# Performance work log

Hardware: AMD Instinct MI355X
Metric: run time of the kernel (lower is better)

The kernel has to match this reference:

```python
import jax, jax.numpy as jnp
import numpy as np

B, S, D, H = 2, 2048, 1024, 16
HD = D // H  # 64
EPS = 1e-8


def setup_inputs() -> dict:
    key = jax.random.key(0)
    ks = jax.random.split(key, 9)
    hidden_states = jax.random.normal(ks[0], (B, S, D), dtype=jnp.float32)
    # rotary tables: standard RoPE angles over half the head dim
    pos = jnp.arange(S, dtype=jnp.float32)[:, None]
    inv_freq = 1.0 / (10000.0 ** (jnp.arange(0, HD, 2, dtype=jnp.float32) / HD))  # [HD/2]
    ang = pos * inv_freq[None, :]  # [S, HD/2]
    sin = jnp.sin(ang)[None, None]  # [1,1,S,HD/2]
    cos = jnp.cos(ang)[None, None]
    s = 1.0 / np.sqrt(D)
    wq = jax.random.normal(ks[1], (D, D), dtype=jnp.float32) * s
    wk = jax.random.normal(ks[2], (D, D), dtype=jnp.float32) * s
    wv = jax.random.normal(ks[3], (D, D), dtype=jnp.float32) * s
    wo = jax.random.normal(ks[4], (D, D), dtype=jnp.float32) * s
    bo = jnp.zeros((D,), dtype=jnp.float32)
    scale = jnp.ones((D,), dtype=jnp.float32)
    return {"hidden_states": hidden_states, "sin": sin, "cos": cos,
            "wq": wq, "wk": wk, "wv": wv, "wo": wo, "bo": bo, "scale": scale}


def _heads(x):
    # [B,S,D] -> [B,H,S,HD]
    return x.reshape(B, S, H, HD).transpose(0, 2, 1, 3)


def _rotary(x, sin, cos):
    # interleaved RoPE: even/odd pairs
    x1, x2 = x[..., 0::2], x[..., 1::2]
    out = jnp.stack([x1 * cos - x2 * sin, x2 * cos + x1 * sin], axis=-1)
    return out.reshape(x.shape)


def reference(hidden_states, sin, cos, wq, wk, wv, wo, bo, scale):
    q = _rotary(_heads(hidden_states @ wq.T), sin, cos)
    k = _rotary(_heads(hidden_states @ wk.T), sin, cos)
    v = _rotary(_heads(hidden_states @ wv.T), sin, cos)
    scores = jnp.einsum("bhqd,bhkd->bhqk", q, k) / np.sqrt(HD)
    probs = jax.nn.softmax(scores, axis=-1)
    ctx = jnp.einsum("bhqk,bhkd->bhqd", probs, v)
    ctx = ctx.transpose(0, 2, 1, 3).reshape(B, S, D)
    out = ctx @ wo.T + bo
    x = out + hidden_states
    # RMSNorm: x / (||x||/sqrt(d) + eps) * scale
    rms = jnp.linalg.norm(x, axis=-1, keepdims=True) / np.sqrt(D)
    return scale * (x / (rms + EPS))
```

## Files before the change

kernel.cpp:

```cpp
#include <hip/hip_runtime.h>
#include <cmath>

#define BB 2
#define SS 2048
#define DD 1024
#define HH 16
#define HDIM 64
#define KDIM 1024
#define EPSF 1e-8f
#define QSCALE 0.18033688f

typedef __attribute__((ext_vector_type(8))) short bf16x8;
typedef __attribute__((ext_vector_type(4))) float f32x4;
typedef __attribute__((ext_vector_type(16))) float f32x16;

__device__ __forceinline__ ushort f2bf(float x) {
    unsigned u = __builtin_bit_cast(unsigned, x);
    u += 0x7FFFu + ((u >> 16) & 1u);
    return (ushort)(u >> 16);
}

__device__ __forceinline__ unsigned pack_bf16_trunc(float a, float b) {
    return __builtin_amdgcn_perm(__builtin_bit_cast(unsigned, b),
                                 __builtin_bit_cast(unsigned, a), 0x07060302u);
}

__device__ __forceinline__ float exp2_fast(float x) {
    float r;
    asm("v_exp_f32 %0, %1" : "=v"(r) : "v"(x));
    return r;
}

__device__ __forceinline__ void gload_lds16(const ushort* g, ushort* l) {
    __builtin_amdgcn_global_load_lds(
        (const __attribute__((address_space(1))) unsigned*)g,
        (__attribute__((address_space(3))) unsigned*)l, 16, 0, 0);
}

__global__ __launch_bounds__(256) void conv_all(
    const float* __restrict__ hs, const float* __restrict__ wq,
    const float* __restrict__ wk, const float* __restrict__ wv,
    const float* __restrict__ wo, ushort* __restrict__ dst)
{
    const int i = blockIdx.x * 256 + threadIdx.x;
    const int HS4 = (BB * SS * DD) / 4;
    const int W4 = (DD * DD) / 4;
    const float* src;
    int off;
    if (i < HS4) { src = hs; off = i; }
    else {
        const int j = i - HS4;
        const int seg = j / W4;
        off = j - seg * W4;
        src = (seg == 0) ? wq : (seg == 1) ? wk : (seg == 2) ? wv : wo;
    }
    const float4 v = ((const float4*)src)[off];
    ushort4 o;
    o.x = f2bf(v.x); o.y = f2bf(v.y); o.z = f2bf(v.z); o.w = f2bf(v.w);
    ((ushort4*)dst)[i] = o;
}

__global__ __launch_bounds__(256) void gemm_qkv_mfma(
    const ushort* __restrict__ A,
    const ushort* __restrict__ Wq, const ushort* __restrict__ Wk,
    const ushort* __restrict__ Wv,
    const float* __restrict__ sinp, const float* __restrict__ cosp,
    ushort* __restrict__ Qb, ushort* __restrict__ Kb, ushort* __restrict__ Vtb)
{
    const int cb = blockIdx.y;
    const int z = cb >> 3;
    const int col0 = (cb & 7) * 128;
    const ushort* W = (z == 0) ? Wq : (z == 1) ? Wk : Wv;
    ushort* O = (z == 0) ? Qb : (z == 1) ? Kb : Vtb;
    const int row0 = blockIdx.x * 128;
    const float qs = (z == 0) ? QSCALE : 1.0f;

    __shared__ __align__(16) ushort As[128 * 32];
    __shared__ __align__(16) ushort Bs[128 * 32];

    const int tid = threadIdx.x;
    const int w = tid >> 6, lane = tid & 63;
    const int quad = lane >> 4, l15 = lane & 15;
    const int m_off = (w >> 1) * 64, n_off = (w & 1) * 64;

    f32x4 acc[4][4] = {};

    for (int k0 = 0; k0 < KDIM; k0 += 32) {
#pragma unroll
        for (int it = 0; it < 2; ++it) {
            const int L = (it * 4 + w) * 64 + lane;
            const int r = L >> 2, c8 = (L & 3) * 8;
            gload_lds16(A + (size_t)(row0 + r) * KDIM + k0 + c8, &As[L * 8]);
            gload_lds16(W + (size_t)(col0 + r) * KDIM + k0 + c8, &Bs[L * 8]);
        }
        __syncthreads();
        bf16x8 af[4], bfr[4];
#pragma unroll
        for (int i = 0; i < 4; ++i) {
            af[i]  = *(const bf16x8*)&As[(m_off + i * 16 + l15) * 32 + quad * 8];
            bfr[i] = *(const bf16x8*)&Bs[(n_off + i * 16 + l15) * 32 + quad * 8];
        }
#pragma unroll
        for (int i = 0; i < 4; ++i)
#pragma unroll
            for (int j = 0; j < 4; ++j)
                acc[i][j] = __builtin_amdgcn_mfma_f32_16x16x32_bf16(
                    af[i], bfr[j], acc[i][j], 0, 0, 0);
        __syncthreads();
    }

    const int b = (row0 + m_off) / SS;
#pragma unroll
    for (int mi = 0; mi < 4; ++mi) {
        const int mrow = row0 + m_off + mi * 16 + quad * 4;
#pragma unroll
        for (int ni = 0; ni < 4; ++ni) {
            const int c = col0 + n_off + ni * 16 + l15;
            const int h = c >> 6, e = c & 63;
            const int bh = b * HH + h;
            float outv[4];
#pragma unroll
            for (int r = 0; r < 4; ++r) {
                const int s = (mrow + r) & (SS - 1);
                const float sv = sinp[s * (HDIM / 2) + (e >> 1)];
                const float cv = cosp[s * (HDIM / 2) + (e >> 1)];
                const float v = acc[mi][ni][r];
                const float vp = __shfl_xor(v, 1);
                outv[r] = ((l15 & 1) ? (v * cv + vp * sv) : (v * cv - vp * sv)) * qs;
            }
            if (z < 2) {
#pragma unroll
                for (int r = 0; r < 4; ++r) {
                    const int s = (mrow + r) & (SS - 1);
                    const ushort mine = f2bf(outv[r]);
                    const ushort part = (ushort)__shfl_xor((int)mine, 1);
                    if (!(l15 & 1))
                        *(unsigned*)(O + ((size_t)(bh * SS + s)) * HDIM + e) =
                            (unsigned)mine | ((unsigned)part << 16);
                }
            } else {
                ushort4 pk;
                pk.x = f2bf(outv[0]); pk.y = f2bf(outv[1]);
                pk.z = f2bf(outv[2]); pk.w = f2bf(outv[3]);
                const int s0 = mrow & (SS - 1);
                *(ushort4*)(O + ((size_t)(bh * HDIM + e)) * SS + s0) = pk;
            }
        }
    }
}

__global__ __launch_bounds__(256) void attn_mfma(
    const ushort* __restrict__ Qb, const ushort* __restrict__ Kb,
    const ushort* __restrict__ Vtb, ushort* __restrict__ ctx)
{
    const int bh = blockIdx.y;
    const int b = bh / HH, h = bh % HH;
    const int q0 = blockIdx.x * 64;
    const int tid = threadIdx.x;
    const int w = tid >> 6;
    const int lane = tid & 63;
    const int l31 = lane & 31;
    const int g = lane >> 5;
    const int strip = w >> 1;
    const int phase = w & 1;

    __shared__ __align__(16) ushort kv[2][2][128][32];

    const ushort* Qh = Qb  + (size_t)bh * SS * HDIM;
    const ushort* Kh = Kb  + (size_t)bh * SS * HDIM;
    const ushort* Vh = Vtb + (size_t)bh * HDIM * SS;

    const int qrow = q0 + strip * 32 + l31;
    bf16x8 qf[4];
#pragma unroll
    for (int ks = 0; ks < 4; ++ks)
        qf[ks] = *(const bf16x8*)(Qh + (size_t)qrow * HDIM + ks * 16 + g * 8);

    f32x16 cacc[2] = {};
    float lsum = 0.f;

    const int lr = lane >> 2;
    const int c16 = lane & 3;
    const int lc = c16 * 8;
    const int swc = (c16 ^ (lr & 3)) * 8;

    union U32x4 { unsigned u[4]; bf16x8 v; };

    uint4 rk00, rk01, rk10, rk11, rv00, rv01, rv10, rv11;

#define LOAD_STAGE(K0)                                                        \
    do {                                                                      \
        const ushort* Kb_ = Kh + (size_t)((K0) + w * 16 + lr) * HDIM + lc;    \
        const ushort* Vb_ = Vh + (size_t)(w * 16 + lr) * SS + (K0) + lc;      \
        rk00 = *(const uint4*)(Kb_);                                          \
        rk01 = *(const uint4*)(Kb_ + 32);                                     \
        rk10 = *(const uint4*)(Kb_ + (size_t)64 * HDIM);                      \
        rk11 = *(const uint4*)(Kb_ + (size_t)64 * HDIM + 32);                 \
        rv00 = *(const uint4*)(Vb_);                                          \
        rv01 = *(const uint4*)(Vb_ + 32);                                     \
        rv10 = *(const uint4*)(Vb_ + 64);                                     \
        rv11 = *(const uint4*)(Vb_ + 96);                                     \
    } while (0)

#define WRITE_STAGE()                                                         \
    do {                                                                      \
        *(uint4*)&kv[0][0][     w * 16 + lr][swc] = rk00;                     \
        *(uint4*)&kv[0][0][64 + w * 16 + lr][swc] = rk01;                     \
        *(uint4*)&kv[1][0][     w * 16 + lr][swc] = rk10;                     \
        *(uint4*)&kv[1][0][64 + w * 16 + lr][swc] = rk11;                     \
        *(uint4*)&kv[0][1][     w * 16 + lr][swc] = rv00;                     \
        *(uint4*)&kv[0][1][64 + w * 16 + lr][swc] = rv01;                     \
        *(uint4*)&kv[1][1][     w * 16 + lr][swc] = rv10;                     \
        *(uint4*)&kv[1][1][64 + w * 16 + lr][swc] = rv11;                     \
    } while (0)


    LOAD_STAGE(0);

    for (int k0 = 0; k0 < SS; k0 += 128) {
        __syncthreads();
        WRITE_STAGE();
        __syncthreads();
        if (k0 + 128 < SS) LOAD_STAGE(k0 + 128);

        f32x16 sacc[2] = {};
#pragma unroll
        for (int kt = 0; kt < 2; ++kt)
#pragma unroll
            for (int ks = 0; ks < 4; ++ks) {
                const int row = kt * 32 + l31;
                const bf16x8 kf = *(const bf16x8*)&kv[phase][0]
                    [(ks >> 1) * 64 + row][(((ks & 1) * 2 + g) ^ (row & 3)) * 8];
                sacc[kt] = __builtin_amdgcn_mfma_f32_32x32x16_bf16(
                    kf, qf[ks], sacc[kt], 0, 0, 0);
            }

        unsigned pk[2][8];
#pragma unroll
        for (int kt = 0; kt < 2; ++kt)
#pragma unroll
            for (int i = 0; i < 8; ++i) {
                const float pa = exp2_fast(sacc[kt][2 * i]);
                const float pb = exp2_fast(sacc[kt][2 * i + 1]);
                lsum += pa + pb;
                pk[kt][i] = pack_bf16_trunc(pa, pb);
            }

#pragma unroll
        for (int ks = 0; ks < 4; ++ks) {
            const int kt = ks >> 1, bq = (ks & 1) * 4;
            const unsigned s0 = (unsigned)__shfl_xor((int)pk[kt][bq + 0], 32);
            const unsigned s1 = (unsigned)__shfl_xor((int)pk[kt][bq + 1], 32);
            const unsigned s2 = (unsigned)__shfl_xor((int)pk[kt][bq + 2], 32);
            const unsigned s3 = (unsigned)__shfl_xor((int)pk[kt][bq + 3], 32);
            U32x4 pf;
            pf.u[0] = g ? s2 : pk[kt][bq + 0];
            pf.u[1] = g ? s3 : pk[kt][bq + 1];
            pf.u[2] = g ? pk[kt][bq + 2] : s0;
            pf.u[3] = g ? pk[kt][bq + 3] : s1;
#pragma unroll
            for (int dt = 0; dt < 2; ++dt) {
                const int row = dt * 32 + l31;
                const bf16x8 vf = *(const bf16x8*)&kv[phase][1]
                    [(ks >> 1) * 64 + row][(((ks & 1) * 2 + g) ^ (row & 3)) * 8];
                cacc[dt] = __builtin_amdgcn_mfma_f32_32x32x16_bf16(
                    vf, pf.v, cacc[dt], 0, 0, 0);
            }
        }
    }

    lsum += __shfl_xor(lsum, 32);

    __syncthreads();
    float* mlds = (float*)kv;
    const int mbase = strip * 2112 + lane * 33;
    if (phase == 1) {
#pragma unroll
        for (int dt = 0; dt < 2; ++dt)
#pragma unroll
            for (int i = 0; i < 16; ++i) mlds[mbase + dt * 16 + i] = cacc[dt][i];
        mlds[mbase + 32] = lsum;
    }
    __syncthreads();
    if (phase == 0) {
#pragma unroll
        for (int dt = 0; dt < 2; ++dt)
#pragma unroll
            for (int i = 0; i < 16; ++i) cacc[dt][i] += mlds[mbase + dt * 16 + i];
        lsum += mlds[mbase + 32];
        const float inv = 1.f / lsum;

        const size_t obase = ((size_t)(b * SS + qrow)) * DD + h * HDIM;
#pragma unroll
        for (int dt = 0; dt < 2; ++dt)
#pragma unroll
            for (int t = 0; t < 4; ++t) {
                ushort4 o;
                o.x = f2bf(cacc[dt][t * 4 + 0] * inv);
                o.y = f2bf(cacc[dt][t * 4 + 1] * inv);
                o.z = f2bf(cacc[dt][t * 4 + 2] * inv);
                o.w = f2bf(cacc[dt][t * 4 + 3] * inv);
                *(ushort4*)(ctx + obase + dt * 32 + t * 8 + g * 4) = o;
            }
    }
#undef LOAD_STAGE
#undef WRITE_STAGE
}

__global__ __launch_bounds__(256) void gemm_out_mfma(
    const ushort* __restrict__ A, const ushort* __restrict__ W,
    const float* __restrict__ bias, float* __restrict__ Out)
{
    const int row0 = blockIdx.x * 128;
    const int col0 = blockIdx.y * 64;

    __shared__ __align__(16) ushort As[128 * 32];
    __shared__ __align__(16) ushort Bs[64 * 32];

    const int tid = threadIdx.x;
    const int w = tid >> 6, lane = tid & 63;
    const int quad = lane >> 4, l15 = lane & 15;
    const int m_off = (w >> 1) * 64, n_off = (w & 1) * 32;

    f32x4 acc[4][2] = {};

    for (int k0 = 0; k0 < KDIM; k0 += 32) {
#pragma unroll
        for (int it = 0; it < 2; ++it) {
            const int L = (it * 4 + w) * 64 + lane;
            const int r = L >> 2, c8 = (L & 3) * 8;
            gload_lds16(A + (size_t)(row0 + r) * KDIM + k0 + c8, &As[L * 8]);
        }
        {
            const int L = w * 64 + lane;
            const int r = L >> 2, c8 = (L & 3) * 8;
            gload_lds16(W + (size_t)(col0 + r) * KDIM + k0 + c8, &Bs[L * 8]);
        }
        __syncthreads();
        bf16x8 af[4], bfr[2];
#pragma unroll
        for (int i = 0; i < 4; ++i)
            af[i] = *(const bf16x8*)&As[(m_off + i * 16 + l15) * 32 + quad * 8];
#pragma unroll
        for (int j = 0; j < 2; ++j)
            bfr[j] = *(const bf16x8*)&Bs[(n_off + j * 16 + l15) * 32 + quad * 8];
#pragma unroll
        for (int i = 0; i < 4; ++i)
#pragma unroll
            for (int j = 0; j < 2; ++j)
                acc[i][j] = __builtin_amdgcn_mfma_f32_16x16x32_bf16(
                    af[i], bfr[j], acc[i][j], 0, 0, 0);
        __syncthreads();
    }

#pragma unroll
    for (int mi = 0; mi < 4; ++mi) {
        const int mrow = row0 + m_off + mi * 16 + quad * 4;
#pragma unroll
        for (int ni = 0; ni < 2; ++ni) {
            const int c = col0 + n_off + ni * 16 + l15;
            const float bv = bias[c];
#pragma unroll
            for (int r = 0; r < 4; ++r)
                Out[(size_t)(mrow + r) * DD + c] = acc[mi][ni][r] + bv;
        }
    }
}

__global__ __launch_bounds__(256) void resid_rmsnorm(
    const float* __restrict__ proj, const float* __restrict__ hs,
    const float* __restrict__ scale, float* __restrict__ out)
{
    const int t = blockIdx.x;
    const int tid = threadIdx.x;
    const size_t base = (size_t)t * DD + tid * 4;

    const float4 p4 = *(const float4*)(proj + base);
    const float4 h4 = *(const float4*)(hs + base);
    float x0 = p4.x + h4.x, x1 = p4.y + h4.y, x2 = p4.z + h4.z, x3 = p4.w + h4.w;
    float ss = x0 * x0 + x1 * x1 + x2 * x2 + x3 * x3;

#pragma unroll
    for (int off = 1; off < 64; off <<= 1) ss += __shfl_xor(ss, off);

    __shared__ float wsum[4];
    if ((tid & 63) == 0) wsum[tid >> 6] = ss;
    __syncthreads();
    const float total = wsum[0] + wsum[1] + wsum[2] + wsum[3];
    const float inv = 1.f / (sqrtf(total * (1.f / DD)) + EPSF);

    const float4 s4 = *(const float4*)(scale + tid * 4);
    float4 o;
    o.x = s4.x * x0 * inv;
    o.y = s4.y * x1 * inv;
    o.z = s4.z * x2 * inv;
    o.w = s4.w * x3 * inv;
    *(float4*)(out + base) = o;
}

extern "C" void kernel_launch(void* const* d_in, const int* in_sizes, int n_in,
                              void* d_out, int out_size, void* d_ws, size_t ws_size,
                              hipStream_t stream) {
    const float* hs    = (const float*)d_in[0];
    const float* sinp  = (const float*)d_in[1];
    const float* cosp  = (const float*)d_in[2];
    const float* wq    = (const float*)d_in[3];
    const float* wk    = (const float*)d_in[4];
    const float* wv    = (const float*)d_in[5];
    const float* wo    = (const float*)d_in[6];
    const float* bo    = (const float*)d_in[7];
    const float* scale = (const float*)d_in[8];
    float* out = (float*)d_out;

    unsigned char* wsb = (unsigned char*)d_ws;
    const size_t MAT = (size_t)BB * SS * DD;
    const size_t WN  = (size_t)DD * DD;
    ushort* Abf = (ushort*)wsb;
    ushort* Wqb = Abf + MAT;
    ushort* Wkb = Wqb + WN;
    ushort* Wvb = Wkb + WN;
    ushort* Wob = Wvb + WN;
    ushort* Qb  = Wob + WN;
    ushort* Kb  = Qb + MAT;
    ushort* Vtb = Kb + MAT;
    ushort* ctxb = Vtb + MAT;
    float* proj = (float*)(ctxb + MAT);

    const int nconv4 = (int)((MAT + 4 * WN) / 4);
    conv_all<<<dim3(nconv4 / 256), 256, 0, stream>>>(hs, wq, wk, wv, wo, Abf);

    gemm_qkv_mfma<<<dim3(32, 24), 256, 0, stream>>>(Abf, Wqb, Wkb, Wvb,
                                                    sinp, cosp, Qb, Kb, Vtb);
    attn_mfma<<<dim3(SS / 64, BB * HH), 256, 0, stream>>>(Qb, Kb, Vtb, ctxb);
    gemm_out_mfma<<<dim3(32, 16), 256, 0, stream>>>(ctxb, Wob, bo, proj);
    resid_rmsnorm<<<dim3(BB * SS), 256, 0, stream>>>(proj, hs, scale, out);
}
```

Before: 218.3 us.

## Double-buffer attention KV tiles in LDS and remap blocks per XCD

Measured after the change: 213.9 us. 2.0% less time.

```diff
diff --git a/kernel.cpp b/kernel.cpp
--- a/kernel.cpp
+++ b/kernel.cpp
@@ -153,9 +153,12 @@
     const ushort* __restrict__ Qb, const ushort* __restrict__ Kb,
     const ushort* __restrict__ Vtb, ushort* __restrict__ ctx)
 {
-    const int bh = blockIdx.y;
+    const int wg  = blockIdx.x;
+    const int lin = (wg & 7) * 128 + (wg >> 3);
+    const int bh   = lin >> 5;
+    const int qblk = lin & 31;
     const int b = bh / HH, h = bh % HH;
-    const int q0 = blockIdx.x * 64;
+    const int q0 = qblk * 64;
     const int tid = threadIdx.x;
     const int w = tid >> 6;
     const int lane = tid & 63;
@@ -164,7 +167,7 @@
     const int strip = w >> 1;
     const int phase = w & 1;
 
-    __shared__ __align__(16) ushort kv[2][2][128][32];
+    __shared__ __align__(16) ushort kvb[2][2][2][64][32];
 
     const ushort* Qh = Qb  + (size_t)bh * SS * HDIM;
     const ushort* Kh = Kb  + (size_t)bh * SS * HDIM;
@@ -183,96 +186,89 @@
     const int c16 = lane & 3;
     const int lc = c16 * 8;
     const int swc = (c16 ^ (lr & 3)) * 8;
-
-    union U32x4 { unsigned u[4]; bf16x8 v; };
-
-    uint4 rk00, rk01, rk10, rk11, rv00, rv01, rv10, rv11;
+    const int srow = w * 16 + lr;
+
+    uint4 rk0, rk1, rv0, rv1;
 
 #define LOAD_STAGE(K0)                                                        \
     do {                                                                      \
-        const ushort* Kb_ = Kh + (size_t)((K0) + w * 16 + lr) * HDIM + lc;    \
-        const ushort* Vb_ = Vh + (size_t)(w * 16 + lr) * SS + (K0) + lc;      \
-        rk00 = *(const uint4*)(Kb_);                                          \
-        rk01 = *(const uint4*)(Kb_ + 32);                                     \
-        rk10 = *(const uint4*)(Kb_ + (size_t)64 * HDIM);                      \
-        rk11 = *(const uint4*)(Kb_ + (size_t)64 * HDIM + 32);                 \
-        rv00 = *(const uint4*)(Vb_);                                          \
-        rv01 = *(const uint4*)(Vb_ + 32);                                     \
-        rv10 = *(const uint4*)(Vb_ + 64);                                     \
-        rv11 = *(const uint4*)(Vb_ + 96);                                     \
+        const ushort* Kp = Kh + (size_t)((K0) + srow) * HDIM + lc;            \
+        const ushort* Vp = Vh + (size_t)srow * SS + (K0) + lc;                \
+        rk0 = *(const uint4*)(Kp);                                            \
+        rk1 = *(const uint4*)(Kp + 32);                                       \
+        rv0 = *(const uint4*)(Vp);                                            \
+        rv1 = *(const uint4*)(Vp + 32);                                       \
     } while (0)
 
-#define WRITE_STAGE()                                                         \
+#define WRITE_STAGE(bufi)                                                     \
     do {                                                                      \
-        *(uint4*)&kv[0][0][     w * 16 + lr][swc] = rk00;                     \
-        *(uint4*)&kv[0][0][64 + w * 16 + lr][swc] = rk01;                     \
-        *(uint4*)&kv[1][0][     w * 16 + lr][swc] = rk10;                     \
-        *(uint4*)&kv[1][0][64 + w * 16 + lr][swc] = rk11;                     \
-        *(uint4*)&kv[0][1][     w * 16 + lr][swc] = rv00;                     \
-        *(uint4*)&kv[0][1][64 + w * 16 + lr][swc] = rv01;                     \
-        *(uint4*)&kv[1][1][     w * 16 + lr][swc] = rv10;                     \
-        *(uint4*)&kv[1][1][64 + w * 16 + lr][swc] = rv11;                     \
+        *(uint4*)&kvb[bufi][0][0][srow][swc] = rk0;                           \
+        *(uint4*)&kvb[bufi][0][1][srow][swc] = rk1;                           \
+        *(uint4*)&kvb[bufi][1][0][srow][swc] = rv0;                           \
+        *(uint4*)&kvb[bufi][1][1][srow][swc] = rv1;                           \
     } while (0)
 
+    const int NT = SS / 64;
 
     LOAD_STAGE(0);
-
-    for (int k0 = 0; k0 < SS; k0 += 128) {
+    WRITE_STAGE(0);
+    LOAD_STAGE(64);
+
+    for (int t = 0; t < NT; ++t) {
         __syncthreads();
-        WRITE_STAGE();
-        __syncthreads();
-        if (k0 + 128 < SS) LOAD_STAGE(k0 + 128);
-
-        f32x16 sacc[2] = {};
-#pragma unroll
-        for (int kt = 0; kt < 2; ++kt)
-#pragma unroll
-            for (int ks = 0; ks < 4; ++ks) {
-                const int row = kt * 32 + l31;
-                const bf16x8 kf = *(const bf16x8*)&kv[phase][0]
-                    [(ks >> 1) * 64 + row][(((ks & 1) * 2 + g) ^ (row & 3)) * 8];
-                sacc[kt] = __builtin_amdgcn_mfma_f32_32x32x16_bf16(
-                    kf, qf[ks], sacc[kt], 0, 0, 0);
-            }
-
-        unsigned pk[2][8];
-#pragma unroll
-        for (int kt = 0; kt < 2; ++kt)
-#pragma unroll
-            for (int i = 0; i < 8; ++i) {
-                const float pa = exp2_fast(sacc[kt][2 * i]);
-                const float pb = exp2_fast(sacc[kt][2 * i + 1]);
-                lsum += pa + pb;
-                pk[kt][i] = pack_bf16_trunc(pa, pb);
-            }
-
-#pragma unroll
-        for (int ks = 0; ks < 4; ++ks) {
-            const int kt = ks >> 1, bq = (ks & 1) * 4;
-            const unsigned s0 = (unsigned)__shfl_xor((int)pk[kt][bq + 0], 32);
-            const unsigned s1 = (unsigned)__shfl_xor((int)pk[kt][bq + 1], 32);
-            const unsigned s2 = (unsigned)__shfl_xor((int)pk[kt][bq + 2], 32);
-            const unsigned s3 = (unsigned)__shfl_xor((int)pk[kt][bq + 3], 32);
-            U32x4 pf;
-            pf.u[0] = g ? s2 : pk[kt][bq + 0];
-            pf.u[1] = g ? s3 : pk[kt][bq + 1];
-            pf.u[2] = g ? pk[kt][bq + 2] : s0;
-            pf.u[3] = g ? pk[kt][bq + 3] : s1;
+        const int cur = t & 1;
+
+        bf16x8 kf[4];
+#pragma unroll
+        for (int ks = 0; ks < 4; ++ks)
+            kf[ks] = *(const bf16x8*)&kvb[cur][0][ks >> 1]
+                [phase * 32 + l31][(((ks & 1) * 2 + g) ^ (l31 & 3)) * 8];
+
+        if (t + 1 < NT) WRITE_STAGE(cur ^ 1);
+        if (t + 2 < NT) LOAD_STAGE((t + 2) * 64);
+
+        f32x16 sacc = {};
+        __builtin_amdgcn_s_setprio(1);
+#pragma unroll
+        for (int ks = 0; ks < 4; ++ks)
+            sacc = __builtin_amdgcn_mfma_f32_32x32x16_bf16(
+                kf[ks], qf[ks], sacc, 0, 0, 0);
+        __builtin_amdgcn_s_setprio(0);
+
+        unsigned pk[8];
+#pragma unroll
+        for (int i = 0; i < 8; ++i) {
+            const float pa = exp2_fast(sacc[2 * i]);
+            const float pb = exp2_fast(sacc[2 * i + 1]);
+            lsum += pa + pb;
+            pk[i] = pack_bf16_trunc(pa, pb);
+        }
+
+#pragma unroll
+        for (int ks = 0; ks < 2; ++ks) {
+            const int bq = ks * 4;
+            unsigned a0 = pk[bq + 0], a1 = pk[bq + 1];
+            unsigned b0 = pk[bq + 2], b1 = pk[bq + 3];
+            asm("v_permlane32_swap_b32 %0, %1" : "+v"(a0), "+v"(b0));
+            asm("v_permlane32_swap_b32 %0, %1" : "+v"(a1), "+v"(b1));
+            union { unsigned u[4]; bf16x8 v; } pf;
+            pf.u[0] = a0; pf.u[1] = a1; pf.u[2] = b0; pf.u[3] = b1;
+            __builtin_amdgcn_s_setprio(1);
 #pragma unroll
             for (int dt = 0; dt < 2; ++dt) {
-                const int row = dt * 32 + l31;
-                const bf16x8 vf = *(const bf16x8*)&kv[phase][1]
-                    [(ks >> 1) * 64 + row][(((ks & 1) * 2 + g) ^ (row & 3)) * 8];
+                const bf16x8 vf = *(const bf16x8*)&kvb[cur][1][phase]
+                    [dt * 32 + l31][((ks * 2 + g) ^ (l31 & 3)) * 8];
                 cacc[dt] = __builtin_amdgcn_mfma_f32_32x32x16_bf16(
                     vf, pf.v, cacc[dt], 0, 0, 0);
             }
+            __builtin_amdgcn_s_setprio(0);
         }
     }
 
     lsum += __shfl_xor(lsum, 32);
 
     __syncthreads();
-    float* mlds = (float*)kv;
+    float* mlds = (float*)kvb;
     const int mbase = strip * 2112 + lane * 33;
     if (phase == 1) {
 #pragma unroll
@@ -431,7 +427,7 @@
 
     gemm_qkv_mfma<<<dim3(32, 24), 256, 0, stream>>>(Abf, Wqb, Wkb, Wvb,
                                                     sinp, cosp, Qb, Kb, Vtb);
-    attn_mfma<<<dim3(SS / 64, BB * HH), 256, 0, stream>>>(Qb, Kb, Vtb, ctxb);
+    attn_mfma<<<dim3(32 * BB * HH), 256, 0, stream>>>(Qb, Kb, Vtb, ctxb);
     gemm_out_mfma<<<dim3(32, 16), 256, 0, stream>>>(ctxb, Wob, bo, proj);
     resid_rmsnorm<<<dim3(BB * SS), 256, 0, stream>>>(proj, hs, scale, out);
 }
```
